# Kernel tuning notes

Measured on AMD Instinct MI355X. Metric: run time of the kernel, lower is better.

Reference implementation:

```python
import jax, jax.numpy as jnp
import numpy as np

D_MODEL = 1024
D_FF = 4096
N_HEADS = 16
HEAD_DIM = D_MODEL // N_HEADS
EPS = 1e-6
B, S = 4, 2048


def _linear_params(key, d_in, d_out):
    kw, kb = jax.random.split(key)
    scale = 1.0 / np.sqrt(d_in)
    w = jax.random.uniform(kw, (d_in, d_out), minval=-scale, maxval=scale, dtype=jnp.float32)
    b = jax.random.uniform(kb, (d_out,), minval=-scale, maxval=scale, dtype=jnp.float32)
    return w, b


def setup_inputs() -> dict:
    key = jax.random.key(0)
    ks = jax.random.split(key, 16)
    x = jax.random.normal(ks[0], (B, S, D_MODEL), dtype=jnp.float32)
    enc = jax.random.normal(ks[1], (B, S, D_MODEL), dtype=jnp.float32)
    # masked self-attention params
    wq1, bq1 = _linear_params(ks[2], D_MODEL, D_MODEL)
    wk1, bk1 = _linear_params(ks[3], D_MODEL, D_MODEL)
    wv1, bv1 = _linear_params(ks[4], D_MODEL, D_MODEL)
    wo1, bo1 = _linear_params(ks[5], D_MODEL, D_MODEL)
    # cross-attention params
    wq2, bq2 = _linear_params(ks[6], D_MODEL, D_MODEL)
    wk2, bk2 = _linear_params(ks[7], D_MODEL, D_MODEL)
    wv2, bv2 = _linear_params(ks[8], D_MODEL, D_MODEL)
    wo2, bo2 = _linear_params(ks[9], D_MODEL, D_MODEL)
    # feed-forward params
    wf1, bf1 = _linear_params(ks[10], D_MODEL, D_FF)
    wf2, bf2 = _linear_params(ks[11], D_FF, D_MODEL)
    # layer norms
    g1 = jnp.ones((D_MODEL,), jnp.float32); be1 = jnp.zeros((D_MODEL,), jnp.float32)
    g2 = jnp.ones((D_MODEL,), jnp.float32); be2 = jnp.zeros((D_MODEL,), jnp.float32)
    g3 = jnp.ones((D_MODEL,), jnp.float32); be3 = jnp.zeros((D_MODEL,), jnp.float32)
    return dict(x=x, encoder_output=enc,
                wq1=wq1, bq1=bq1, wk1=wk1, bk1=bk1, wv1=wv1, bv1=bv1, wo1=wo1, bo1=bo1,
                wq2=wq2, bq2=bq2, wk2=wk2, bk2=bk2, wv2=wv2, bv2=bv2, wo2=wo2, bo2=bo2,
                wf1=wf1, bf1=bf1, wf2=wf2, bf2=bf2,
                g1=g1, be1=be1, g2=g2, be2=be2, g3=g3, be3=be3)


def _layer_norm(x, g, b):
    mu = jnp.mean(x, axis=-1, keepdims=True)
    var = jnp.mean(jnp.square(x - mu), axis=-1, keepdims=True)
    return (x - mu) * jax.lax.rsqrt(var + EPS) * g + b


def _mha(q_in, k_in, v_in, wq, bq, wk, bk, wv, bv, wo, bo, causal):
    b, s, _ = q_in.shape
    q = (q_in @ wq + bq).reshape(b, s, N_HEADS, HEAD_DIM)
    k = (k_in @ wk + bk).reshape(b, -1, N_HEADS, HEAD_DIM)
    v = (v_in @ wv + bv).reshape(b, -1, N_HEADS, HEAD_DIM)
    scores = jnp.einsum('bqhd,bkhd->bhqk', q, k) / np.sqrt(HEAD_DIM)
    if causal:
        mask = jnp.tril(jnp.ones((s, s), dtype=bool))
        scores = jnp.where(mask, scores, jnp.finfo(scores.dtype).min)
    attn = jax.nn.softmax(scores, axis=-1)
    out = jnp.einsum('bhqk,bkhd->bqhd', attn, v).reshape(b, s, D_MODEL)
    return out @ wo + bo


def reference(x, encoder_output,
              wq1, bq1, wk1, bk1, wv1, bv1, wo1, bo1,
              wq2, bq2, wk2, bk2, wv2, bv2, wo2, bo2,
              wf1, bf1, wf2, bf2,
              g1, be1, g2, be2, g3, be3):
    # masked self-attention + residual + LN
    residual = x
    x = _mha(x, x, x, wq1, bq1, wk1, bk1, wv1, bv1, wo1, bo1, causal=True)
    x = _layer_norm(x + residual, g1, be1)
    # cross-attention (note: q=enc, k=enc, v=x as in the original) + residual + LN
    residual = x
    x = _mha(encoder_output, encoder_output, x, wq2, bq2, wk2, bk2, wv2, bv2, wo2, bo2, causal=False)
    x = _layer_norm(x + residual, g2, be2)
    # feed-forward (dropout=0 -> identity in eval) + residual + LN
    residual = x
    x = jax.nn.relu(x @ wf1 + bf1) @ wf2 + bf2
    x = _layer_norm(x + residual, g3, be3)
    return x
```

## Files before the change

### kernel.cpp

```cpp
#include <hip/hip_runtime.h>


typedef _Float16 f16;
typedef _Float16 f16x8 __attribute__((ext_vector_type(8)));
typedef _Float16 f16x4 __attribute__((ext_vector_type(4)));
typedef __fp16 fp16x2 __attribute__((ext_vector_type(2)));
typedef float f32x4 __attribute__((ext_vector_type(4)));
typedef float f32x16 __attribute__((ext_vector_type(16)));
typedef unsigned int u32;

#define AS1 __attribute__((address_space(1)))
#define AS3 __attribute__((address_space(3)))

constexpr int S_LEN = 2048;
constexpr int DM    = 1024;

constexpr long OFF_W    = 0;
constexpr long OFF_XB   = 32L  << 20;
constexpr long OFF_ENC  = 48L  << 20;
constexpr long OFF_Q    = 64L  << 20;
constexpr long OFF_K    = 80L  << 20;
constexpr long OFF_V    = 96L  << 20;
constexpr long OFF_VT   = 112L << 20;
constexpr long OFF_AC   = 128L << 20;
constexpr long OFF_HID  = 144L << 20;
constexpr long OFF_F2   = 240L << 20;
constexpr long OFF_PART = 304L << 20;
constexpr long BUF_BYTES = 336L << 20;

__device__ alignas(4096) unsigned char g_buf[BUF_BYTES];

constexpr long WQ1T = OFF_W + (0L  << 20);
constexpr long WF1T = OFF_W + (16L << 20);
constexpr long WF2T = OFF_W + (24L << 20);
constexpr long WO1T = OFF_W + (6L  << 20);
constexpr long WQ2T = OFF_W + (8L  << 20);
constexpr long WV2T = OFF_W + (12L << 20);
constexpr long WO2T = OFF_W + (14L << 20);

__global__ __launch_bounds__(256) void cvt2_k(const float* __restrict__ x,
                                              const float* __restrict__ enc)
{
    const int bid = blockIdx.x;
    const bool second = bid >= 8192;
    const float* in = second ? enc : x;
    f16* out = (f16*)(g_buf + (second ? OFF_ENC : OFF_XB));
    long i = (long)(second ? bid - 8192 : bid) * 256 + threadIdx.x;
    float4 v = ((const float4*)in)[i];
    f16x4 h;
    h[0] = (f16)v.x; h[1] = (f16)v.y; h[2] = (f16)v.z; h[3] = (f16)v.w;
    *(f16x4*)(out + i * 4) = h;
}

struct TWJobs { const float* src[10]; };

__global__ __launch_bounds__(256) void transw_all_k(TWJobs jobs)
{
    __shared__ float t[32][33];
    const int bid = blockIdx.x;
    int j, local;
    if (bid < 8192)       { j = bid >> 10; local = bid & 1023; }
    else if (bid < 12288) { j = 8; local = bid - 8192; }
    else                  { j = 9; local = bid - 12288; }
    const int K = (j == 9) ? 4096 : 1024;
    const int N = (j == 8) ? 4096 : 1024;
    const int tnx = N >> 5;
    const int tx32 = local % tnx, ty32 = local / tnx;
    const long dstOff = (j < 8) ? (long)j * (2L << 20) : ((j == 8) ? WF1T : WF2T);
    const float* W = jobs.src[j];
    f16* Wt = (f16*)(g_buf + dstOff);

    int tx = threadIdx.x, ty = threadIdx.y;
    int c0 = tx32 * 32, r0 = ty32 * 32;
#pragma unroll
    for (int i = 0; i < 4; ++i)
        t[ty + 8*i][tx] = W[(long)(r0 + ty + 8*i) * N + c0 + tx];
    __syncthreads();
#pragma unroll
    for (int i = 0; i < 4; ++i)
        Wt[(long)(c0 + ty + 8*i) * K + r0 + tx] = (f16)t[tx][ty + 8*i];
}

template<int MODE>
__global__ __launch_bounds__(256) void gemm3_k(
    long aOff, long bOff, long cOff, long vtOff,
    const float* __restrict__ b0, const float* __restrict__ b1,
    const float* __restrict__ b2, const float* __restrict__ b3,
    int K, int lda, int ldb, int ldc, long chunkStride, int tvch)
{
    __shared__ alignas(16) f16 As[3][128 * 32];
    __shared__ alignas(16) f16 Bs[3][128 * 32];

    const int tid  = threadIdx.x;
    const int lane = tid & 63;
    const int w    = tid >> 6;
    const int cB   = lane & 15;
    const int hi   = lane >> 4;

    const int nwg = gridDim.x * gridDim.y;
    const int id  = blockIdx.y * gridDim.x + blockIdx.x;
    const int swz = (id & 7) * (nwg >> 3) + (id >> 3);
    const int bx  = swz % gridDim.x, by = swz / gridDim.x;
    const int row0 = by * 128, col0 = bx * 128;

    const f16* Ab = (const f16*)(g_buf + aOff);
    const f16* Bb = (const f16*)(g_buf + bOff);

    const int wr = (w >> 1) * 64;
    const int wc = (w & 1) * 64;

    f32x4 acc[4][4] = {};

    auto stage = [&](int buf, int kt) {
        const int kB = kt * 32;
        const int base = w * 64;
#pragma unroll
        for (int r = 0; r < 2; ++r) {
            const int idx  = r * 256 + base + lane;
            const int srow = idx >> 2, sb = idx & 3;
            const int gk = (sb ^ ((srow >> 1) & 3)) << 3;
            __builtin_amdgcn_global_load_lds(
                (const AS1 void*)(Ab + (long)(row0 + srow) * lda + kB + gk),
                (AS3 void*)(&As[buf][(r * 256 + base) * 8]), 16, 0, 0);
            __builtin_amdgcn_global_load_lds(
                (const AS1 void*)(Bb + (long)(col0 + srow) * ldb + kB + gk),
                (AS3 void*)(&Bs[buf][(r * 256 + base) * 8]), 16, 0, 0);
        }
    };

    const int nt = K >> 5;
    stage(0, 0);
    stage(1, 1);

    for (int t = 0; t < nt; ++t) {
        if (nt - t >= 2) asm volatile("s_waitcnt vmcnt(4)" ::: "memory");
        else             asm volatile("s_waitcnt vmcnt(0)" ::: "memory");
        __builtin_amdgcn_s_barrier();
        __builtin_amdgcn_sched_barrier(0);
        if (t + 2 < nt) stage((t + 2) % 3, t + 2);

        const int cur = t % 3;
        f16x8 af[4], bf[4];
#pragma unroll
        for (int m = 0; m < 4; ++m) {
            const int row = wr + m * 16 + cB;
            af[m] = *(const f16x8*)&As[cur][row * 32 + ((hi ^ ((row >> 1) & 3)) << 3)];
        }
#pragma unroll
        for (int n = 0; n < 4; ++n) {
            const int row = wc + n * 16 + cB;
            bf[n] = *(const f16x8*)&Bs[cur][row * 32 + ((hi ^ ((row >> 1) & 3)) << 3)];
        }
        __builtin_amdgcn_s_setprio(1);
#pragma unroll
        for (int m = 0; m < 4; ++m)
#pragma unroll
            for (int n = 0; n < 4; ++n)
                acc[m][n] = __builtin_amdgcn_mfma_f32_16x16x32_f16(af[m], bf[n], acc[m][n], 0, 0, 0);
        __builtin_amdgcn_s_setprio(0);
    }

    const int ch = col0 >> 10;
    const float* bp = (ch == 0) ? b0 : (ch == 1) ? b1 : (ch == 2) ? b2 : b3;

    if (MODE == 0 && ch == tvch) {
        f16* Vt = (f16*)(g_buf + vtOff);
#pragma unroll
        for (int m = 0; m < 4; ++m) {
#pragma unroll
            for (int n = 0; n < 4; ++n) {
                const int c = col0 + wc + n * 16 + cB;
                const int hh = (c >> 6) & 15, dd = c & 63;
                const float bv = bp[c & 1023];
                const int r0e = row0 + wr + m * 16 + hi * 4;
                const int bb = r0e >> 11, sS = r0e & 2047;
                f16x4 hv;
#pragma unroll
                for (int jj = 0; jj < 4; ++jj) hv[jj] = (f16)(acc[m][n][jj] + bv);
                *(f16x4*)(Vt + (((long)(bb * 16 + hh) * 64 + dd) * 2048 + sS)) = hv;
            }
        }
        return;
    }

    float* Cf = (float*)(g_buf + cOff);
    f16*  Ch = (f16*)(g_buf + cOff);
    const long cBase = (long)ch * chunkStride;
#pragma unroll
    for (int m = 0; m < 4; ++m) {
#pragma unroll
        for (int n = 0; n < 4; ++n) {
            const int c = col0 + wc + n * 16 + cB;
            const float bv = bp[c & 1023];
#pragma unroll
            for (int jj = 0; jj < 4; ++jj) {
                const int r = row0 + wr + m * 16 + hi * 4 + jj;
                float v = acc[m][n][jj] + bv;
                const long idx = cBase + (long)r * ldc + (c & 1023);
                if constexpr (MODE == 2) Cf[idx] = v;
                else                     Ch[idx] = (f16)v;
            }
        }
    }
}

template<int MODE>
__global__ __launch_bounds__(512, 1) void gemm8_k(
    long aOff, long bOff, long cOff, long partOff, long vtOff,
    const float* __restrict__ b0, const float* __restrict__ b1,
    const float* __restrict__ b2, const float* __restrict__ b3,
    int K, int lda, int ldb, int ldc, long chunkStride, int tvch)
{
    __shared__ alignas(16) f16 As[2][2][8192];
    __shared__ alignas(16) f16 Bs[2][2][8192];

    const int tid  = threadIdx.x;
    const int lane = tid & 63;
    const int w    = tid >> 6;
    const int cB   = lane & 15;
    const int hi   = lane >> 4;

    const int gx = gridDim.x, gy = gridDim.y;
    const int nwg = gx * gy * gridDim.z;
    const int id  = ((int)blockIdx.z * gy + (int)blockIdx.y) * gx + (int)blockIdx.x;
    const int swz = (id & 7) * (nwg >> 3) + (id >> 3);
    const int bx  = swz % gx;
    const int rem = swz / gx;
    const int by  = rem % gy;
    const int bz  = rem / gy;
    const int row0 = by * 256, col0 = bx * 256;

    const f16* Ab = (const f16*)(g_buf + aOff) + (long)bz * K;
    const f16* Bb = (const f16*)(g_buf + bOff) + (long)bz * K;

    const int wr = (w >> 2) * 128;
    const int wc = (w & 3) * 64;

    f32x4 acc[8][4] = {};

    auto stagePlane = [&](int buf, int kt, int mat, int kh) {
        const int kB = kt * 64 + kh * 32;
        const f16* src = mat ? Bb : Ab;
        const int ld   = mat ? ldb : lda;
        const int r0g  = mat ? col0 : row0;
        f16* dst = mat ? &Bs[buf][kh][0] : &As[buf][kh][0];
#pragma unroll
        for (int r = 0; r < 2; ++r) {
            const int idx  = r * 512 + w * 64 + lane;
            const int srow = idx >> 2, sb = idx & 3;
            const int gk = (sb ^ ((srow >> 1) & 3)) << 3;
            __builtin_amdgcn_global_load_lds(
                (const AS1 void*)(src + (long)(r0g + srow) * ld + kB + gk),
                (AS3 void*)(dst + (r * 512 + w * 64) * 8), 16, 0, 0);
        }
    };

    auto rdA = [&](int buf, int kh, int mf) -> f16x8 {
        const int row = wr + mf * 16 + cB;
        return *(const f16x8*)&As[buf][kh][row * 32 + ((hi ^ ((row >> 1) & 3)) << 3)];
    };
    auto rdB = [&](int buf, int kh, int nf) -> f16x8 {
        const int row = wc + nf * 16 + cB;
        return *(const f16x8*)&Bs[buf][kh][row * 32 + ((hi ^ ((row >> 1) & 3)) << 3)];
    };

    const int nt = K >> 6;
    stagePlane(0, 0, 0, 0);
    stagePlane(0, 0, 1, 0);
    stagePlane(0, 0, 0, 1);
    stagePlane(0, 0, 1, 1);

    for (int t = 0; t < nt; ++t) {
        const int cur = t & 1, nxt = cur ^ 1;
        const bool pf = (t + 1 < nt);
        f16x8 a[4], b[4];

        asm volatile("s_waitcnt vmcnt(4)" ::: "memory");
        __builtin_amdgcn_s_barrier();
        __builtin_amdgcn_sched_barrier(0);
#pragma unroll
        for (int n = 0; n < 4; ++n) b[n] = rdB(cur, 0, n);
#pragma unroll
        for (int m = 0; m < 4; ++m) a[m] = rdA(cur, 0, m);
        if (pf) stagePlane(nxt, t + 1, 0, 0);
        asm volatile("s_waitcnt lgkmcnt(0)" ::: "memory");
        __builtin_amdgcn_sched_barrier(0);
        __builtin_amdgcn_s_setprio(1);
#pragma unroll
        for (int m = 0; m < 4; ++m)
#pragma unroll
            for (int n = 0; n < 4; ++n)
                acc[m][n] = __builtin_amdgcn_mfma_f32_16x16x32_f16(a[m], b[n], acc[m][n], 0, 0, 0);
        __builtin_amdgcn_s_setprio(0);

        __builtin_amdgcn_s_barrier();
        __builtin_amdgcn_sched_barrier(0);
#pragma unroll
        for (int m = 0; m < 4; ++m) a[m] = rdA(cur, 0, m + 4);
        if (pf) stagePlane(nxt, t + 1, 1, 0);
        asm volatile("s_waitcnt lgkmcnt(0)" ::: "memory");
        __builtin_amdgcn_sched_barrier(0);
        __builtin_amdgcn_s_setprio(1);
#pragma unroll
        for (int m = 0; m < 4; ++m)
#pragma unroll
            for (int n = 0; n < 4; ++n)
                acc[4 + m][n] = __builtin_amdgcn_mfma_f32_16x16x32_f16(a[m], b[n], acc[4 + m][n], 0, 0, 0);
        __builtin_amdgcn_s_setprio(0);

        if (pf) asm volatile("s_waitcnt vmcnt(4)" ::: "memory");
        else    asm volatile("s_waitcnt vmcnt(0)" ::: "memory");
        __builtin_amdgcn_s_barrier();
        __builtin_amdgcn_sched_barrier(0);
#pragma unroll
        for (int n = 0; n < 4; ++n) b[n] = rdB(cur, 1, n);
#pragma unroll
        for (int m = 0; m < 4; ++m) a[m] = rdA(cur, 1, m);
        if (pf) stagePlane(nxt, t + 1, 0, 1);
        asm volatile("s_waitcnt lgkmcnt(0)" ::: "memory");
        __builtin_amdgcn_sched_barrier(0);
        __builtin_amdgcn_s_setprio(1);
#pragma unroll
        for (int m = 0; m < 4; ++m)
#pragma unroll
            for (int n = 0; n < 4; ++n)
                acc[m][n] = __builtin_amdgcn_mfma_f32_16x16x32_f16(a[m], b[n], acc[m][n], 0, 0, 0);
        __builtin_amdgcn_s_setprio(0);

        __builtin_amdgcn_s_barrier();
        __builtin_amdgcn_sched_barrier(0);
#pragma unroll
        for (int m = 0; m < 4; ++m) a[m] = rdA(cur, 1, m + 4);
        if (pf) stagePlane(nxt, t + 1, 1, 1);
        asm volatile("s_waitcnt lgkmcnt(0)" ::: "memory");
        __builtin_amdgcn_sched_barrier(0);
        __builtin_amdgcn_s_setprio(1);
#pragma unroll
        for (int m = 0; m < 4; ++m)
#pragma unroll
            for (int n = 0; n < 4; ++n)
                acc[4 + m][n] = __builtin_amdgcn_mfma_f32_16x16x32_f16(a[m], b[n], acc[4 + m][n], 0, 0, 0);
        __builtin_amdgcn_s_setprio(0);
    }

    const int ch = col0 >> 10;
    const float* bp = (ch == 0) ? b0 : (ch == 1) ? b1 : (ch == 2) ? b2 : b3;

    if (MODE == 0 && ch == tvch) {
        f16* Vt = (f16*)(g_buf + vtOff);
#pragma unroll
        for (int m = 0; m < 8; ++m) {
#pragma unroll
            for (int n = 0; n < 4; ++n) {
                const int c = col0 + wc + n * 16 + cB;
                const int hh = (c >> 6) & 15, dd = c & 63;
                const float bv = bp[c & 1023];
                const int r0e = row0 + wr + m * 16 + hi * 4;
                const int bb = r0e >> 11, sS = r0e & 2047;
                f16x4 hv;
#pragma unroll
                for (int jj = 0; jj < 4; ++jj) hv[jj] = (f16)(acc[m][n][jj] + bv);
                *(f16x4*)(Vt + (((long)(bb * 16 + hh) * 64 + dd) * 2048 + sS)) = hv;
            }
        }
        return;
    }

    float* Cf = (float*)(g_buf + (bz ? partOff : cOff));
    f16*  Ch = (f16*)(g_buf + cOff);
    const long cBase = (long)ch * chunkStride;
#pragma unroll
    for (int m = 0; m < 8; ++m) {
#pragma unroll
        for (int n = 0; n < 4; ++n) {
            const int c = col0 + wc + n * 16 + cB;
            const float bv = bz ? 0.f : bp[c & 1023];
#pragma unroll
            for (int jj = 0; jj < 4; ++jj) {
                const int r = row0 + wr + m * 16 + hi * 4 + jj;
                float v = acc[m][n][jj] + bv;
                if constexpr (MODE == 1) v = fmaxf(v, 0.f);
                const long idx = cBase + (long)r * ldc + (c & 1023);
                if constexpr (MODE == 2) Cf[idx] = v;
                else                     Ch[idx] = (f16)v;
            }
        }
    }
}

template<int CAUSAL>
__global__ __launch_bounds__(512, 2) void flash_k(long qOff, long kOff, long vtOff, long oOff)
{
    __shared__ alignas(16) f16 SH[32768];

    const int tid  = threadIdx.x;
    const int lane = tid & 63;
    const int w    = tid >> 6;
    const int ql   = lane & 31;
    const int s    = lane >> 5;

    const int raw   = (int)blockIdx.y * (int)gridDim.x + (int)blockIdx.x;
    const int newid = (raw & 7) * 64 + (raw >> 3);
    const int bh    = newid >> 3;
    const int p     = newid & 7;

    const int qt  = CAUSAL ? ((w >> 2) ? 15 - p : p) : (2 * p + (w >> 2));
    const int q0w = qt * 128 + (w & 3) * 32;
    const int nch = CAUSAL ? (16 - p) : 16;

    const int b = bh >> 4, h = bh & 15;
    const long tokB = (long)b * S_LEN;

    const f16* Qb  = (const f16*)(g_buf + qOff);
    const f16* Kb  = (const f16*)(g_buf + kOff);
    const f16* Vtb = (const f16*)(g_buf + vtOff) + (long)bh * 64 * S_LEN;
    f16* Ob = (f16*)(g_buf + oOff);

    const int r8  = lane >> 3;
    const int c8  = lane & 7;
    const int sbK = c8 ^ r8;
    const int d16 = lane >> 4;
    const int b16 = lane & 15;

    auto stage = [&](int buf, int c) {
        const int kv0s = c * 128;
#pragma unroll
        for (int r = 0; r < 2; ++r) {
            const int row = w * 16 + r * 8 + r8;
            __builtin_amdgcn_global_load_lds(
                (const AS1 void*)(Kb + (tokB + kv0s + row) * DM + h * 64 + sbK * 8),
                (AS3 void*)(&SH[buf * 16384 + (w * 16 + r * 8) * 64]), 16, 0, 0);
        }
#pragma unroll
        for (int r = 0; r < 2; ++r) {
            const int d = w * 8 + r * 4 + d16;
            __builtin_amdgcn_global_load_lds(
                (const AS1 void*)(Vtb + (long)d * S_LEN + kv0s + (b16 ^ (d & 7)) * 8),
                (AS3 void*)(&SH[buf * 16384 + 8192 + (w * 8 + r * 4) * 128]), 16, 0, 0);
        }
    };

    stage(0, 0);

    f16x8 qf[4];
    {
        const f16 hs = (f16)(0.125f * 1.44269504088896f);
        const f16* qrow = Qb + (tokB + q0w + ql) * DM + h * 64 + s * 8;
#pragma unroll
        for (int kk = 0; kk < 4; ++kk) {
            qf[kk] = *(const f16x8*)(qrow + kk * 16);
#pragma unroll
            for (int i = 0; i < 8; ++i) qf[kk][i] = qf[kk][i] * hs;
        }
    }

    f32x16 oacc[2] = {};
    float lrow = 0.f;

    for (int c = 0; c < nch; ++c) {
        const int cur = c & 1;

        asm volatile("s_waitcnt vmcnt(0) lgkmcnt(0)" ::: "memory");
        __builtin_amdgcn_sched_barrier(0);
        __builtin_amdgcn_s_barrier();
        __builtin_amdgcn_sched_barrier(0);
        if (c + 1 < nch) stage(cur ^ 1, c + 1);

        const char* Kl = (const char*)SH + cur * 32768;
        const char* Vl = Kl + 16384;

#pragma unroll
        for (int sub = 0; sub < 2; ++sub) {
            const int kv0 = c * 128 + sub * 64;
            const bool active = !CAUSAL || (kv0 <= q0w + 31);
            if (!active) continue;

            f32x16 pr[2] = {};
            __builtin_amdgcn_s_setprio(1);
#pragma unroll
            for (int kk = 0; kk < 4; ++kk) {
                const int t16 = (kk * 2 + s) ^ (ql & 7);
                f16x8 kf0 = *(const f16x8*)(Kl + (sub * 64 + ql) * 128 + t16 * 16);
                f16x8 kf1 = *(const f16x8*)(Kl + (sub * 64 + 32 + ql) * 128 + t16 * 16);
                pr[0] = __builtin_amdgcn_mfma_f32_32x32x16_f16(kf0, qf[kk], pr[0], 0, 0, 0);
                pr[1] = __builtin_amdgcn_mfma_f32_32x32x16_f16(kf1, qf[kk], pr[1], 0, 0, 0);
            }
            __builtin_amdgcn_s_setprio(0);

            if (CAUSAL && (kv0 + 63 > q0w)) {
                const int q = q0w + ql;
#pragma unroll
                for (int v = 0; v < 2; ++v)
#pragma unroll
                    for (int r = 0; r < 16; ++r) {
                        const int kv = kv0 + v * 32 + (r & 3) + 8 * (r >> 2) + 4 * s;
                        if (kv > q) pr[v][r] = -1e30f;
                    }
            }

            u32 pk[2][4][2];
            float rp[4] = {0.f, 0.f, 0.f, 0.f};
#pragma unroll
            for (int v = 0; v < 2; ++v)
#pragma unroll
                for (int a = 0; a < 4; ++a)
#pragma unroll
                    for (int cc = 0; cc < 2; ++cc) {
                        const float e0 = __builtin_amdgcn_exp2f(pr[v][4 * a + 2 * cc] - 8.0f);
                        const float e1 = __builtin_amdgcn_exp2f(pr[v][4 * a + 2 * cc + 1] - 8.0f);
                        rp[a] += e0 + e1;
                        union { fp16x2 h; u32 u; } cv;
                        cv.h = __builtin_amdgcn_cvt_pkrtz(e0, e1);
                        pk[v][a][cc] = cv.u;
                    }
            float rsum = (rp[0] + rp[1]) + (rp[2] + rp[3]);
            rsum += __shfl_xor(rsum, 32);
            lrow += rsum;

            u32 loc[2][2][2], exv[2][2][2];
#pragma unroll
            for (int v = 0; v < 2; ++v)
#pragma unroll
                for (int k1 = 0; k1 < 2; ++k1)
#pragma unroll
                    for (int cc = 0; cc < 2; ++cc) {
                        const u32 pe = pk[v][2 * k1][cc];
                        const u32 po = pk[v][2 * k1 + 1][cc];
                        loc[v][k1][cc] = s ? po : pe;
                        const u32 snd = s ? pe : po;
                        exv[v][k1][cc] = (u32)__shfl_xor((int)snd, 32);
                    }

            __builtin_amdgcn_s_setprio(1);
#pragma unroll
            for (int ks = 0; ks < 4; ++ks) {
                const int v = ks >> 1, k1 = ks & 1;
                union { u32 u[4]; f16x8 hv; } pa;
                pa.u[0] = s ? exv[v][k1][0] : loc[v][k1][0];
                pa.u[1] = s ? exv[v][k1][1] : loc[v][k1][1];
                pa.u[2] = s ? loc[v][k1][0] : exv[v][k1][0];
                pa.u[3] = s ? loc[v][k1][1] : exv[v][k1][1];
                const int tv = sub * 8 + ((ks * 2 + s) ^ (ql & 7));
                f16x8 vf0 = *(const f16x8*)(Vl + ql * 256 + tv * 16);
                f16x8 vf1 = *(const f16x8*)(Vl + (32 + ql) * 256 + tv * 16);
                oacc[0] = __builtin_amdgcn_mfma_f32_32x32x16_f16(pa.hv, vf0, oacc[0], 0, 0, 0);
                oacc[1] = __builtin_amdgcn_mfma_f32_32x32x16_f16(pa.hv, vf1, oacc[1], 0, 0, 0);
            }
            __builtin_amdgcn_s_setprio(0);
        }
    }

    asm volatile("s_waitcnt lgkmcnt(0)" ::: "memory");
    __builtin_amdgcn_sched_barrier(0);
    __builtin_amdgcn_s_barrier();

    f16* Es = SH + w * 2304;
    const float linv = 1.0f / lrow;
#pragma unroll
    for (int r = 0; r < 16; ++r) {
        const int qr = (r & 3) + 8 * (r >> 2) + 4 * s;
        const float lb = __shfl(linv, qr);
        Es[qr * 72 + ql]      = (f16)(oacc[0][r] * lb);
        Es[qr * 72 + 32 + ql] = (f16)(oacc[1][r] * lb);
    }
    const int orow = lane >> 1;
    const int oh   = (lane & 1) * 32;
    const f16* srcp = Es + orow * 72 + oh;
    f16* dst = Ob + (tokB + q0w + orow) * DM + h * 64 + oh;
#pragma unroll
    for (int t = 0; t < 4; ++t)
        *(f16x8*)(dst + t * 8) = *(const f16x8*)(srcp + t * 8);
}

__global__ __launch_bounds__(256) void ln_k(
    long inOff, long in2Off, const float* __restrict__ residF, long residHOff,
    const float* __restrict__ gamma, const float* __restrict__ beta,
    float* __restrict__ outFExt, long outHOff)
{
    const float* in = (const float*)(g_buf + inOff);

    const long row = blockIdx.x;
    const int tid = threadIdx.x;
    const int lane = tid & 63, wid = tid >> 6;

    float4 a = ((const float4*)(in + row * DM))[tid];
    float x0 = a.x, x1 = a.y, x2 = a.z, x3 = a.w;
    if (residF) {
        float4 rr = ((const float4*)(residF + row * DM))[tid];
        x0 += rr.x; x1 += rr.y; x2 += rr.z; x3 += rr.w;
    }
    if (residHOff >= 0) {
        const f16* rh = (const f16*)(g_buf + residHOff) + row * DM + tid * 4;
        f16x4 rv = *(const f16x4*)rh;
        x0 += (float)rv[0]; x1 += (float)rv[1]; x2 += (float)rv[2]; x3 += (float)rv[3];
    }
    if (in2Off >= 0) {
        const float* in2 = (const float*)(g_buf + in2Off);
        float4 p = ((const float4*)(in2 + row * DM))[tid];
        x0 += p.x; x1 += p.y; x2 += p.z; x3 += p.w;
    }

    __shared__ float red[4];
    float ss = x0 + x1 + x2 + x3;
#pragma unroll
    for (int o = 32; o > 0; o >>= 1) ss += __shfl_xor(ss, o);
    if (lane == 0) red[wid] = ss;
    __syncthreads();
    const float mu = (red[0] + red[1] + red[2] + red[3]) * (1.0f / DM);

    float d0 = x0 - mu, d1 = x1 - mu, d2 = x2 - mu, d3 = x3 - mu;
    float qq = d0*d0 + d1*d1 + d2*d2 + d3*d3;
#pragma unroll
    for (int o = 32; o > 0; o >>= 1) qq += __shfl_xor(qq, o);
    __syncthreads();
    if (lane == 0) red[wid] = qq;
    __syncthreads();
    const float var = (red[0] + red[1] + red[2] + red[3]) * (1.0f / DM);
    const float rs = rsqrtf(var + 1e-6f);

    float4 g  = ((const float4*)gamma)[tid];
    float4 be = ((const float4*)beta)[tid];
    float y0 = d0 * rs * g.x + be.x;
    float y1 = d1 * rs * g.y + be.y;
    float y2 = d2 * rs * g.z + be.z;
    float y3 = d3 * rs * g.w + be.w;

    if (outFExt)
        ((float4*)(outFExt + row * DM))[tid] = make_float4(y0, y1, y2, y3);
    if (outHOff >= 0) {
        f16* outH = (f16*)(g_buf + outHOff);
        f16x4 hh; hh[0] = (f16)y0; hh[1] = (f16)y1; hh[2] = (f16)y2; hh[3] = (f16)y3;
        *(f16x4*)(outH + row * DM + tid * 4) = hh;
    }
}

extern "C" void kernel_launch(void* const* d_in, const int* in_sizes, int n_in,
                              void* d_out, int out_size, void* d_ws, size_t ws_size,
                              hipStream_t stream)
{
    (void)in_sizes; (void)n_in; (void)d_ws; (void)ws_size; (void)out_size;
    const float* x   = (const float*)d_in[0];
    const float* enc = (const float*)d_in[1];
    const float* wq1 = (const float*)d_in[2];  const float* bq1 = (const float*)d_in[3];
    const float* wk1 = (const float*)d_in[4];  const float* bk1 = (const float*)d_in[5];
    const float* wv1 = (const float*)d_in[6];  const float* bv1 = (const float*)d_in[7];
    const float* wo1 = (const float*)d_in[8];  const float* bo1 = (const float*)d_in[9];
    const float* wq2 = (const float*)d_in[10]; const float* bq2 = (const float*)d_in[11];
    const float* wk2 = (const float*)d_in[12]; const float* bk2 = (const float*)d_in[13];
    const float* wv2 = (const float*)d_in[14]; const float* bv2 = (const float*)d_in[15];
    const float* wo2 = (const float*)d_in[16]; const float* bo2 = (const float*)d_in[17];
    const float* wf1 = (const float*)d_in[18]; const float* bf1 = (const float*)d_in[19];
    const float* wf2 = (const float*)d_in[20]; const float* bf2 = (const float*)d_in[21];
    const float* g1  = (const float*)d_in[22]; const float* be1 = (const float*)d_in[23];
    const float* g2  = (const float*)d_in[24]; const float* be2 = (const float*)d_in[25];
    const float* g3  = (const float*)d_in[26]; const float* be3 = (const float*)d_in[27];
    float* out = (float*)d_out;

    const dim3 T256(256), T512(512), T32x8(32, 8);
    const long QKV_CHUNK = 8192L * 1024;

    cvt2_k<<<16384, T256, 0, stream>>>(x, enc);
    TWJobs jobs;
    jobs.src[0] = wq1; jobs.src[1] = wk1; jobs.src[2] = wv1; jobs.src[3] = wo1;
    jobs.src[4] = wq2; jobs.src[5] = wk2; jobs.src[6] = wv2; jobs.src[7] = wo2;
    jobs.src[8] = wf1; jobs.src[9] = wf2;
    transw_all_k<<<16384, T32x8, 0, stream>>>(jobs);

    gemm8_k<0><<<dim3(12, 32, 1), T512, 0, stream>>>(OFF_XB, WQ1T, OFF_Q, 0, OFF_VT,
        bq1, bk1, bv1, bv1, 1024, 1024, 1024, 1024, QKV_CHUNK, 2);
    flash_k<1><<<dim3(8, 64), T512, 0, stream>>>(OFF_Q, OFF_K, OFF_VT, OFF_AC);
    gemm3_k<2><<<dim3(8, 64), T256, 0, stream>>>(OFF_AC, WO1T, OFF_F2, 0,
        bo1, bo1, bo1, bo1, 1024, 1024, 1024, 1024, 1024, -1);
    ln_k<<<8192, T256, 0, stream>>>(OFF_F2, -1, x, -1, g1, be1, nullptr, OFF_XB);

    gemm8_k<0><<<dim3(8, 32, 1), T512, 0, stream>>>(OFF_ENC, WQ2T, OFF_Q, 0, 0,
        bq2, bk2, bk2, bk2, 1024, 1024, 1024, 1024, QKV_CHUNK, -1);
    gemm3_k<0><<<dim3(8, 64), T256, 0, stream>>>(OFF_XB, WV2T, OFF_V, OFF_VT,
        bv2, bv2, bv2, bv2, 1024, 1024, 1024, 1024, 1024, 0);
    flash_k<0><<<dim3(8, 64), T512, 0, stream>>>(OFF_Q, OFF_K, OFF_VT, OFF_AC);
    gemm3_k<2><<<dim3(8, 64), T256, 0, stream>>>(OFF_AC, WO2T, OFF_F2, 0,
        bo2, bo2, bo2, bo2, 1024, 1024, 1024, 1024, 1024, -1);
    ln_k<<<8192, T256, 0, stream>>>(OFF_F2, -1, nullptr, OFF_XB, g2, be2, nullptr, OFF_XB);

    gemm8_k<1><<<dim3(16, 32, 1), T512, 0, stream>>>(OFF_XB, WF1T, OFF_HID, 0, 0,
        bf1, bf1 + 1024, bf1 + 2048, bf1 + 3072, 1024, 1024, 1024, 4096, 1024, -1);
    gemm8_k<2><<<dim3(4, 32, 2), T512, 0, stream>>>(OFF_HID, WF2T, OFF_F2, OFF_PART, 0,
        bf2, bf2, bf2, bf2, 2048, 4096, 4096, 1024, 1024, -1);
    ln_k<<<8192, T256, 0, stream>>>(OFF_F2, OFF_PART, nullptr, OFF_XB, g3, be3, out, -1);
}
```

Baseline: 580.9 us.

## Restructure 256x256 GEMM into 4-stage K=32 LDS pipeline with 3-tile prefetch

Replaces the double-buffered K=64 pipeline (two K-halves, four barriers per iteration) with a 4-deep ring of K=32 tiles, issuing loads three tiles ahead and synchronising once per tile. The aim is to hide global-to-LDS latency better and cut barriers per unit of MFMA work. LDS use stays the same (4 buffers of 32 columns each for A and B). The trade-off is twice as many loop iterations and waitcnt bookkeeping, and the barrier that protected the ring slot reused by the prefetch now relies on the slot-distance ordering.

Measured after the change: 615.7 us. 6.0% more time.

```diff
diff --git a/kernel.cpp b/kernel.cpp
--- a/kernel.cpp
+++ b/kernel.cpp
@@ -205,14 +205,14 @@
 }
 
 template<int MODE>
-__global__ __launch_bounds__(512, 1) void gemm8_k(
+__global__ __launch_bounds__(512, 1) void gemm9_k(
     long aOff, long bOff, long cOff, long partOff, long vtOff,
     const float* __restrict__ b0, const float* __restrict__ b1,
     const float* __restrict__ b2, const float* __restrict__ b3,
     int K, int lda, int ldb, int ldc, long chunkStride, int tvch)
 {
-    __shared__ alignas(16) f16 As[2][2][8192];
-    __shared__ alignas(16) f16 Bs[2][2][8192];
+    __shared__ alignas(16) f16 As[4][8192];
+    __shared__ alignas(16) f16 Bs[4][8192];
 
     const int tid  = threadIdx.x;
     const int lane = tid & 63;
@@ -238,51 +238,56 @@
 
     f32x4 acc[8][4] = {};
 
-    auto stagePlane = [&](int buf, int kt, int mat, int kh) {
-        const int kB = kt * 64 + kh * 32;
-        const f16* src = mat ? Bb : Ab;
-        const int ld   = mat ? ldb : lda;
-        const int r0g  = mat ? col0 : row0;
-        f16* dst = mat ? &Bs[buf][kh][0] : &As[buf][kh][0];
+    auto stageTile = [&](int buf, int kt) {
+        const int kB = kt * 32;
 #pragma unroll
         for (int r = 0; r < 2; ++r) {
             const int idx  = r * 512 + w * 64 + lane;
             const int srow = idx >> 2, sb = idx & 3;
             const int gk = (sb ^ ((srow >> 1) & 3)) << 3;
             __builtin_amdgcn_global_load_lds(
-                (const AS1 void*)(src + (long)(r0g + srow) * ld + kB + gk),
-                (AS3 void*)(dst + (r * 512 + w * 64) * 8), 16, 0, 0);
+                (const AS1 void*)(Ab + (long)(row0 + srow) * lda + kB + gk),
+                (AS3 void*)(&As[buf][(r * 512 + w * 64) * 8]), 16, 0, 0);
+        }
+#pragma unroll
+        for (int r = 0; r < 2; ++r) {
+            const int idx  = r * 512 + w * 64 + lane;
+            const int srow = idx >> 2, sb = idx & 3;
+            const int gk = (sb ^ ((srow >> 1) & 3)) << 3;
+            __builtin_amdgcn_global_load_lds(
+                (const AS1 void*)(Bb + (long)(col0 + srow) * ldb + kB + gk),
+                (AS3 void*)(&Bs[buf][(r * 512 + w * 64) * 8]), 16, 0, 0);
         }
     };
 
-    auto rdA = [&](int buf, int kh, int mf) -> f16x8 {
+    auto rdA = [&](int buf, int mf) -> f16x8 {
         const int row = wr + mf * 16 + cB;
-        return *(const f16x8*)&As[buf][kh][row * 32 + ((hi ^ ((row >> 1) & 3)) << 3)];
+        return *(const f16x8*)&As[buf][row * 32 + ((hi ^ ((row >> 1) & 3)) << 3)];
     };
-    auto rdB = [&](int buf, int kh, int nf) -> f16x8 {
+    auto rdB = [&](int buf, int nf) -> f16x8 {
         const int row = wc + nf * 16 + cB;
-        return *(const f16x8*)&Bs[buf][kh][row * 32 + ((hi ^ ((row >> 1) & 3)) << 3)];
+        return *(const f16x8*)&Bs[buf][row * 32 + ((hi ^ ((row >> 1) & 3)) << 3)];
     };
 
-    const int nt = K >> 6;
-    stagePlane(0, 0, 0, 0);
-    stagePlane(0, 0, 1, 0);
-    stagePlane(0, 0, 0, 1);
-    stagePlane(0, 0, 1, 1);
+    const int nt = K >> 5;
+    stageTile(0, 0);
+    stageTile(1, 1);
+    stageTile(2, 2);
 
     for (int t = 0; t < nt; ++t) {
-        const int cur = t & 1, nxt = cur ^ 1;
-        const bool pf = (t + 1 < nt);
-        f16x8 a[4], b[4];
-
-        asm volatile("s_waitcnt vmcnt(4)" ::: "memory");
+        const int cur = t & 3;
+        if (t <= nt - 3)      asm volatile("s_waitcnt vmcnt(8)" ::: "memory");
+        else if (t == nt - 2) asm volatile("s_waitcnt vmcnt(4)" ::: "memory");
+        else                  asm volatile("s_waitcnt vmcnt(0)" ::: "memory");
         __builtin_amdgcn_s_barrier();
         __builtin_amdgcn_sched_barrier(0);
-#pragma unroll
-        for (int n = 0; n < 4; ++n) b[n] = rdB(cur, 0, n);
-#pragma unroll
-        for (int m = 0; m < 4; ++m) a[m] = rdA(cur, 0, m);
-        if (pf) stagePlane(nxt, t + 1, 0, 0);
+
+        f16x8 a[4], b[4];
+#pragma unroll
+        for (int n = 0; n < 4; ++n) b[n] = rdB(cur, n);
+#pragma unroll
+        for (int m = 0; m < 4; ++m) a[m] = rdA(cur, m);
+        if (t + 3 < nt) stageTile((t + 3) & 3, t + 3);
         asm volatile("s_waitcnt lgkmcnt(0)" ::: "memory");
         __builtin_amdgcn_sched_barrier(0);
         __builtin_amdgcn_s_setprio(1);
@@ -292,46 +297,10 @@
             for (int n = 0; n < 4; ++n)
                 acc[m][n] = __builtin_amdgcn_mfma_f32_16x16x32_f16(a[m], b[n], acc[m][n], 0, 0, 0);
         __builtin_amdgcn_s_setprio(0);
-
-        __builtin_amdgcn_s_barrier();
         __builtin_amdgcn_sched_barrier(0);
-#pragma unroll
-        for (int m = 0; m < 4; ++m) a[m] = rdA(cur, 0, m + 4);
-        if (pf) stagePlane(nxt, t + 1, 1, 0);
-        asm volatile("s_waitcnt lgkmcnt(0)" ::: "memory");
-        __builtin_amdgcn_sched_barrier(0);
-        __builtin_amdgcn_s_setprio(1);
-#pragma unroll
-        for (int m = 0; m < 4; ++m)
-#pragma unroll
-            for (int n = 0; n < 4; ++n)
-                acc[4 + m][n] = __builtin_amdgcn_mfma_f32_16x16x32_f16(a[m], b[n], acc[4 + m][n], 0, 0, 0);
-        __builtin_amdgcn_s_setprio(0);
-
-        if (pf) asm volatile("s_waitcnt vmcnt(4)" ::: "memory");
-        else    asm volatile("s_waitcnt vmcnt(0)" ::: "memory");
-        __builtin_amdgcn_s_barrier();
-        __builtin_amdgcn_sched_barrier(0);
-#pragma unroll
-        for (int n = 0; n < 4; ++n) b[n] = rdB(cur, 1, n);
-#pragma unroll
-        for (int m = 0; m < 4; ++m) a[m] = rdA(cur, 1, m);
-        if (pf) stagePlane(nxt, t + 1, 0, 1);
-        asm volatile("s_waitcnt lgkmcnt(0)" ::: "memory");
-        __builtin_amdgcn_sched_barrier(0);
-        __builtin_amdgcn_s_setprio(1);
-#pragma unroll
-        for (int m = 0; m < 4; ++m)
-#pragma unroll
-            for (int n = 0; n < 4; ++n)
-                acc[m][n] = __builtin_amdgcn_mfma_f32_16x16x32_f16(a[m], b[n], acc[m][n], 0, 0, 0);
-        __builtin_amdgcn_s_setprio(0);
-
-        __builtin_amdgcn_s_barrier();
-        __builtin_amdgcn_sched_barrier(0);
-#pragma unroll
-        for (int m = 0; m < 4; ++m) a[m] = rdA(cur, 1, m + 4);
-        if (pf) stagePlane(nxt, t + 1, 1, 1);
+
+#pragma unroll
+        for (int m = 0; m < 4; ++m) a[m] = rdA(cur, m + 4);
         asm volatile("s_waitcnt lgkmcnt(0)" ::: "memory");
         __builtin_amdgcn_sched_barrier(0);
         __builtin_amdgcn_s_setprio(1);
@@ -666,14 +635,14 @@
     jobs.src[8] = wf1; jobs.src[9] = wf2;
     transw_all_k<<<16384, T32x8, 0, stream>>>(jobs);
 
-    gemm8_k<0><<<dim3(12, 32, 1), T512, 0, stream>>>(OFF_XB, WQ1T, OFF_Q, 0, OFF_VT,
+    gemm9_k<0><<<dim3(12, 32, 1), T512, 0, stream>>>(OFF_XB, WQ1T, OFF_Q, 0, OFF_VT,
         bq1, bk1, bv1, bv1, 1024, 1024, 1024, 1024, QKV_CHUNK, 2);
     flash_k<1><<<dim3(8, 64), T512, 0, stream>>>(OFF_Q, OFF_K, OFF_VT, OFF_AC);
     gemm3_k<2><<<dim3(8, 64), T256, 0, stream>>>(OFF_AC, WO1T, OFF_F2, 0,
         bo1, bo1, bo1, bo1, 1024, 1024, 1024, 1024, 1024, -1);
     ln_k<<<8192, T256, 0, stream>>>(OFF_F2, -1, x, -1, g1, be1, nullptr, OFF_XB);
 
-    gemm8_k<0><<<dim3(8, 32, 1), T512, 0, stream>>>(OFF_ENC, WQ2T, OFF_Q, 0, 0,
+    gemm9_k<0><<<dim3(8, 32, 1), T512, 0, stream>>>(OFF_ENC, WQ2T, OFF_Q, 0, 0,
         bq2, bk2, bk2, bk2, 1024, 1024, 1024, 1024, QKV_CHUNK, -1);
     gemm3_k<0><<<dim3(8, 64), T256, 0, stream>>>(OFF_XB, WV2T, OFF_V, OFF_VT,
         bv2, bv2, bv2, bv2, 1024, 1024, 1024, 1024, 1024, 0);
@@ -682,9 +651,9 @@
         bo2, bo2, bo2, bo2, 1024, 1024, 1024, 1024, 1024, -1);
     ln_k<<<8192, T256, 0, stream>>>(OFF_F2, -1, nullptr, OFF_XB, g2, be2, nullptr, OFF_XB);
 
-    gemm8_k<1><<<dim3(16, 32, 1), T512, 0, stream>>>(OFF_XB, WF1T, OFF_HID, 0, 0,
+    gemm9_k<1><<<dim3(16, 32, 1), T512, 0, stream>>>(OFF_XB, WF1T, OFF_HID, 0, 0,
         bf1, bf1 + 1024, bf1 + 2048, bf1 + 3072, 1024, 1024, 1024, 4096, 1024, -1);
-    gemm8_k<2><<<dim3(4, 32, 2), T512, 0, stream>>>(OFF_HID, WF2T, OFF_F2, OFF_PART, 0,
+    gemm9_k<2><<<dim3(4, 32, 2), T512, 0, stream>>>(OFF_HID, WF2T, OFF_F2, OFF_PART, 0,
         bf2, bf2, bf2, bf2, 2048, 4096, 4096, 1024, 1024, -1);
     ln_k<<<8192, T256, 0, stream>>>(OFF_F2, OFF_PART, nullptr, OFF_XB, g3, be3, out, -1);
 }
```
